# Kernel optimization log

Measured on AMD Instinct MI355X. Metric: run time of the kernel, lower is better.

Reference implementation:

```python
import jax, jax.numpy as jnp
import numpy as np

NUM_POINTS = 4
MAX_LEVELS = 2


def _bilinear(img, gx, gy, align_corners):
    # img: [C,H,W]; gx,gy: [P] normalized coords in [-1,1]; zero padding (torch grid_sample)
    C, H, W = img.shape
    if align_corners:
        ix = (gx + 1.0) * 0.5 * (W - 1)
        iy = (gy + 1.0) * 0.5 * (H - 1)
    else:
        ix = ((gx + 1.0) * W - 1.0) * 0.5
        iy = ((gy + 1.0) * H - 1.0) * 0.5
    x0 = jnp.floor(ix)
    y0 = jnp.floor(iy)
    wx1 = ix - x0
    wy1 = iy - y0

    def corner(xf, yf, w):
        xi = xf.astype(jnp.int32)
        yi = yf.astype(jnp.int32)
        valid = (xi >= 0) & (xi < W) & (yi >= 0) & (yi < H)
        v = img[:, jnp.clip(yi, 0, H - 1), jnp.clip(xi, 0, W - 1)]  # [C,P]
        return v * (w * valid)[None, :]

    return (corner(x0, y0, (1 - wx1) * (1 - wy1))
            + corner(x0 + 1, y0, wx1 * (1 - wy1))
            + corner(x0, y0 + 1, (1 - wx1) * wy1)
            + corner(x0 + 1, y0 + 1, wx1 * wy1))


_sample_ac = jax.vmap(lambda im, a, b: _bilinear(im, a, b, True))   # warp_affine path
_sample = jax.vmap(lambda im, a, b: _bilinear(im, a, b, False))     # MSDeformAttn path


def _warp_affine(src, M):
    # torch F.affine_grid + F.grid_sample, align_corners=True; src [N,C,H,W], M [N,2,3]
    N, C, H, W = src.shape
    ys = jnp.linspace(-1.0, 1.0, H)
    xs = jnp.linspace(-1.0, 1.0, W)
    gy, gx = jnp.meshgrid(ys, xs, indexing='ij')
    base = jnp.stack([gx.ravel(), gy.ravel(), jnp.ones(H * W, src.dtype)], 0)  # [3,HW]
    grid = jnp.einsum('nij,jp->nip', M, base)  # [N,2,HW]
    return _sample_ac(src, grid[:, 0], grid[:, 1]).reshape(N, C, H, W)


def setup_inputs() -> dict:
    key = jax.random.key(0)
    k = jax.random.split(key, 6)
    B, C, H, W = 2, 256, 100, 252
    x = jax.random.normal(k[0], (4, C, H, W), jnp.float32)
    record_len = jnp.full((B,), 2, dtype=jnp.int32)
    eye = jnp.array([[1.0, 0.0, 0.0], [0.0, 1.0, 0.0]], jnp.float32)
    pairwise_t_matrix = eye + 0.05 * jax.random.normal(k[1], (B, 2, 2, 2, 3), jnp.float32)
    w_off = 0.02 * jax.random.normal(k[2], (C, MAX_LEVELS * NUM_POINTS * 2), jnp.float32)
    b_off = 0.01 * jax.random.normal(k[3], (MAX_LEVELS * NUM_POINTS * 2,), jnp.float32)
    w_attn = 0.02 * jax.random.normal(k[4], (C, MAX_LEVELS * NUM_POINTS), jnp.float32)
    b_attn = 0.01 * jax.random.normal(k[5], (MAX_LEVELS * NUM_POINTS,), jnp.float32)
    return {"x": x, "record_len": record_len, "pairwise_t_matrix": pairwise_t_matrix,
            "w_off": w_off, "b_off": b_off, "w_attn": w_attn, "b_attn": b_attn}


def reference(x, record_len, pairwise_t_matrix, w_off, b_off, w_attn, b_attn):
    rl = [int(v) for v in np.asarray(record_len)]
    C, H, W = x.shape[1:]
    HW = H * W
    # get_reference_points(dim='2d'): pixel centers normalized to (0,1)
    rx = (jnp.arange(W, dtype=x.dtype) + 0.5) / W
    ry = (jnp.arange(H, dtype=x.dtype) + 0.5) / H
    gy, gx = jnp.meshgrid(ry, rx, indexing='ij')
    ref = jnp.stack([gx.ravel(), gy.ravel()], -1)  # [HW,2]
    norm = jnp.array([W, H], dtype=x.dtype)  # offset_normalizer = (W,H) per level
    outs = []
    start = 0
    for b, n in enumerate(rl):
        xx = x[start:start + n]
        start += n
        warped = _warp_affine(xx, pairwise_t_matrix[b, 0, :n])  # [n,C,H,W]
        q = warped[0].reshape(C, HW).T  # query = first agent, [HW,C]
        off = (q @ w_off + b_off).reshape(HW, MAX_LEVELS, NUM_POINTS, 2)[:, :n]  # [HW,n,P,2]
        aw = (q @ w_attn + b_attn).reshape(HW, MAX_LEVELS, NUM_POINTS)[:, :n]
        aw = jax.nn.softmax(aw.reshape(HW, n * NUM_POINTS), axis=-1).reshape(HW, n, NUM_POINTS)
        loc = ref[:, None, None, :] + off / norm  # sampling locations in (0,1)
        grid = 2.0 * loc - 1.0  # [HW,n,P,2]
        gxs = grid[..., 0].transpose(1, 0, 2).reshape(n, HW * NUM_POINTS)
        gys = grid[..., 1].transpose(1, 0, 2).reshape(n, HW * NUM_POINTS)
        sampled = _sample(warped, gxs, gys).reshape(n, C, HW, NUM_POINTS)
        out = jnp.einsum('lcqp,qlp->cq', sampled, aw)  # weighted sum over levels*points
        outs.append(out.reshape(1, C, H, W))
    return jnp.concatenate(outs, 0)
```

## Files before the change

### kernel.cpp

```cpp
#include <hip/hip_runtime.h>
#include <stdint.h>

#define CCH 256
#define NCP 128
#define HH  100
#define WW  252
#define HWSZ (HH*WW)
#define NIMG 4
#define NB   2
#define LP   8

#define TW 64
#define TH 4
#define HLO 2
#define PAIRS_BLOCK 16
#define TILESX ((WW + TW - 1)/TW)
#define TILESY (HH/TH)

#define WRW 70
#define WRH 5
#define WPL 384
#define WISS 6

typedef float vf2 __attribute__((ext_vector_type(2)));

__device__ __forceinline__ uint32_t f2bf(float a) {
  uint32_t u = __float_as_uint(a);
  u += 0x7fffu + ((u >> 16) & 1u);
  return u >> 16;
}
__device__ __forceinline__ float lof(uint32_t u) {
  return __uint_as_float(u << 16);
}
__device__ __forceinline__ float hif(uint32_t u) {
  return __uint_as_float(u & 0xffff0000u);
}
__device__ __forceinline__ vf2 unpk(uint32_t u) {
  vf2 r; r.x = lof(u); r.y = hif(u); return r;
}

__device__ __forceinline__ int swz100(int bid) {
  int xcd = bid & 7, idx = bid >> 3;
  const int q = 100/8, r = 100%8;
  return (xcd < r) ? xcd*(q+1) + idx : r*(q+1) + (xcd-r)*q + idx;
}

__device__ __forceinline__ void gload_lds_u(const uint32_t* g, uint32_t* l) {
  auto gp = reinterpret_cast<const uint32_t __attribute__((address_space(1)))*>(
      reinterpret_cast<uintptr_t>(g));
  auto lp = reinterpret_cast<uint32_t __attribute__((address_space(3)))*>(
      reinterpret_cast<uintptr_t>(l));
  __builtin_amdgcn_global_load_lds(gp, lp, 4, 0, 0);
}

__global__ __launch_bounds__(256) void warp_kernel(
    const float* __restrict__ x, const float* __restrict__ tmat,
    uint32_t* __restrict__ wpk)
{
  int tid = threadIdx.x;
  int y  = swz100(blockIdx.x);
  int g  = blockIdx.y;
  int cc = blockIdx.z;
  bool valid = tid < WW;
  int xo = min(tid, WW-1);
  int b = g >> 1, i = g & 1;
  const float* M = tmat + (size_t)(b*4 + i)*6;
  float m00=M[0], m01=M[1], m02=M[2], m10=M[3], m11=M[4], m12=M[5];
  float gx = -1.0f + 2.0f*(float)xo/(float)(WW-1);
  float gy = -1.0f + 2.0f*(float)y /(float)(HH-1);
  float sx = m00*gx + m01*gy + m02;
  float sy = m10*gx + m11*gy + m12;
  float ix = (sx + 1.0f)*0.5f*(float)(WW-1);
  float iy = (sy + 1.0f)*0.5f*(float)(HH-1);
  float x0f = floorf(ix), y0f = floorf(iy);
  float wx1 = ix - x0f,  wy1 = iy - y0f;
  int x0 = (int)x0f, y0 = (int)y0f;
  int x1 = x0 + 1,  y1 = y0 + 1;
  float v0x = (x0 >= 0 && x0 < WW) ? 1.f : 0.f;
  float v1x = (x1 >= 0 && x1 < WW) ? 1.f : 0.f;
  float v0y = (y0 >= 0 && y0 < HH) ? 1.f : 0.f;
  float v1y = (y1 >= 0 && y1 < HH) ? 1.f : 0.f;
  float w0 = (1.f-wx1)*(1.f-wy1)*v0x*v0y;
  float w1 = wx1*(1.f-wy1)*v1x*v0y;
  float w2 = (1.f-wx1)*wy1*v0x*v1y;
  float w3 = wx1*wy1*v1x*v1y;
  int yc0 = min(max(y0,0),HH-1), yc1 = min(max(y1,0),HH-1);
  int xb  = min(max(x0,0),WW-2);
  bool cnd = (x0 == xb);

  const float* src = x + ((size_t)g*CCH + (size_t)cc*32)*HWSZ;
  uint32_t vo_t = (uint32_t)(yc0*WW + xb)*4u;
  uint32_t vo_b = (uint32_t)(yc1*WW + xb)*4u;
  uint32_t* dst = wpk + ((size_t)g*NCP + (size_t)cc*PAIRS_BLOCK)*HWSZ + y*WW + xo;

  vf2 d[4][4];

  #define WLD(p) do {                                                        \
    uint32_t co = (uint32_t)(2*(p))*(HWSZ*4u);                               \
    asm volatile("global_load_dwordx2 %0, %1, %2"                            \
      : "=v"(d[(p)&3][0]) : "v"(vo_t + co), "s"(src));                       \
    asm volatile("global_load_dwordx2 %0, %1, %2"                            \
      : "=v"(d[(p)&3][1]) : "v"(vo_b + co), "s"(src));                       \
    asm volatile("global_load_dwordx2 %0, %1, %2"                            \
      : "=v"(d[(p)&3][2]) : "v"(vo_t + co + HWSZ*4u), "s"(src));             \
    asm volatile("global_load_dwordx2 %0, %1, %2"                            \
      : "=v"(d[(p)&3][3]) : "v"(vo_b + co + HWSZ*4u), "s"(src));             \
  } while (0)

  #define WCP(p) do {                                                        \
    vf2 t0 = d[(p)&3][0], b0 = d[(p)&3][1];                                  \
    vf2 t1 = d[(p)&3][2], b1 = d[(p)&3][3];                                  \
    float va0 = cnd ? t0.x : t0.y, vb0 = cnd ? t0.y : t0.x;                  \
    float vc0 = cnd ? b0.x : b0.y, vd0 = cnd ? b0.y : b0.x;                  \
    float va1 = cnd ? t1.x : t1.y, vb1 = cnd ? t1.y : t1.x;                  \
    float vc1 = cnd ? b1.x : b1.y, vd1 = cnd ? b1.y : b1.x;                  \
    float v0 = va0*w0 + vb0*w1 + vc0*w2 + vd0*w3;                            \
    float v1 = va1*w0 + vb1*w1 + vc1*w2 + vd1*w3;                            \
    if (valid) dst[(size_t)(p)*HWSZ] = f2bf(v0) | (f2bf(v1) << 16);          \
  } while (0)

  WLD(0); WLD(1); WLD(2); WLD(3);
  #pragma unroll
  for (int p = 0; p < PAIRS_BLOCK; ++p) {
    if      (p == 0)  { asm volatile("s_waitcnt vmcnt(12)" ::: "memory"); }
    else if (p == 1)  { asm volatile("s_waitcnt vmcnt(13)" ::: "memory"); }
    else if (p == 2)  { asm volatile("s_waitcnt vmcnt(14)" ::: "memory"); }
    else if (p <= 12) { asm volatile("s_waitcnt vmcnt(15)" ::: "memory"); }
    else if (p == 13) { asm volatile("s_waitcnt vmcnt(11)" ::: "memory"); }
    else if (p == 14) { asm volatile("s_waitcnt vmcnt(7)"  ::: "memory"); }
    else              { asm volatile("s_waitcnt vmcnt(3)"  ::: "memory"); }
    __builtin_amdgcn_sched_barrier(0);
    WCP(p);
    if (p + 4 < PAIRS_BLOCK) WLD(p + 4);
  }
  #undef WLD
  #undef WCP
}

__global__ __launch_bounds__(256) void b1_kernel(
    const uint32_t* __restrict__ wpk,
    const float* __restrict__ w_off,  const float* __restrict__ b_off,
    const float* __restrict__ w_attn, const float* __restrict__ b_attn,
    float* __restrict__ taps)
{
  __shared__ float red[3][64][25];
  int tid   = threadIdx.x;
  int lpx   = tid & 63;
  int slice = tid >> 6;
  int pix   = blockIdx.x * 64 + lpx;
  int b     = blockIdx.y;
  bool valid = pix < HWSZ;
  int pxc = valid ? pix : (HWSZ-1);
  const uint32_t* q = wpk + ((size_t)(2*b)*NCP + (size_t)slice*32)*HWSZ + pxc;
  float acc[24];
  #pragma unroll
  for (int j=0;j<24;++j) acc[j] = 0.f;
  for (int cp=0; cp<32; ++cp) {
    uint32_t u = q[(size_t)cp*HWSZ];
    float qlo = lof(u), qhi = hif(u);
    int cg = slice*64 + 2*cp;
    #pragma unroll
    for (int j=0;j<16;++j) acc[j]    += qlo * w_off[cg*16+j]  + qhi * w_off[(cg+1)*16+j];
    #pragma unroll
    for (int j=0;j<8;++j)  acc[16+j] += qlo * w_attn[cg*8+j]  + qhi * w_attn[(cg+1)*8+j];
  }
  if (slice > 0) {
    #pragma unroll
    for (int j=0;j<24;++j) red[slice-1][lpx][j] = acc[j];
  }
  __syncthreads();
  if (slice == 0 && valid) {
    #pragma unroll
    for (int s=0;s<3;++s)
      #pragma unroll
      for (int j=0;j<24;++j) acc[j] += red[s][lpx][j];
    #pragma unroll
    for (int j=0;j<16;++j) acc[j]    += b_off[j];
    #pragma unroll
    for (int j=0;j<8;++j)  acc[16+j] += b_attn[j];
    float m = acc[16];
    #pragma unroll
    for (int j=1;j<8;++j) m = fmaxf(m, acc[16+j]);
    float e[8]; float s = 0.f;
    #pragma unroll
    for (int j=0;j<8;++j){ e[j] = __expf(acc[16+j]-m); s += e[j]; }
    float inv = 1.0f/s;
    int px = pix % WW, py = pix / WW;
    float* t = taps + (size_t)b*24*HWSZ + pix;
    #pragma unroll
    for (int k=0;k<LP;++k) {
      t[(size_t)k*HWSZ]      = (float)px + acc[2*k];
      t[(size_t)(8+k)*HWSZ]  = (float)py + acc[2*k+1];
      t[(size_t)(16+k)*HWSZ] = e[k]*inv;
    }
  }
}

__global__ __launch_bounds__(256) void b2_kernel(
    const uint32_t* __restrict__ wpk, const float* __restrict__ taps,
    float* __restrict__ out)
{
  __shared__ uint32_t lds[4*2*2*WPL];
  int tid  = threadIdx.x;
  int lane = tid & 63, wid = tid >> 6;
  int s100 = swz100(blockIdx.x);
  int tx   = s100 / TILESY;
  int ty   = s100 - tx*TILESY;
  int b    = blockIdx.y;
  int pbase = blockIdx.z * PAIRS_BLOCK;
  int tx0 = tx * TW;
  int ty0 = ty * TH;
  int px = tx0 + lane;
  int py = ty0 + wid;
  bool valid = (px < WW);
  int pxc = min(px, WW-1);
  int pix = py*WW + pxc;
  int cx0 = tx0 - HLO;
  int ry0 = py - HLO;

  const float* t = taps + (size_t)b*24*HWSZ + pix;
  float wgt[LP][4];
  int   lidx[LP];
  bool fastall = true;
  #pragma unroll
  for (int k=0;k<LP;++k) {
    float ix = t[(size_t)k*HWSZ];
    float iy = t[(size_t)(8+k)*HWSZ];
    float aw = t[(size_t)(16+k)*HWSZ];
    float x0f = floorf(ix), y0f = floorf(iy);
    float wx1 = ix-x0f, wy1 = iy-y0f;
    int x0=(int)x0f, y0=(int)y0f;
    float v0x = (x0   >= 0 && x0   < WW) ? 1.f : 0.f;
    float v1x = (x0+1 >= 0 && x0+1 < WW) ? 1.f : 0.f;
    float v0y = (y0   >= 0 && y0   < HH) ? 1.f : 0.f;
    float v1y = (y0+1 >= 0 && y0+1 < HH) ? 1.f : 0.f;
    wgt[k][0] = (1.f-wx1)*(1.f-wy1)*v0x*v0y*aw;
    wgt[k][1] = wx1*(1.f-wy1)*v1x*v0y*aw;
    wgt[k][2] = (1.f-wx1)*wy1*v0x*v1y*aw;
    wgt[k][3] = wx1*wy1*v1x*v1y*aw;
    bool f = (x0 >= cx0) && (x0 <= cx0+WRW-2) && (y0 >= ry0) && (y0 <= ry0+WRH-2);
    fastall = fastall && f;
    int li = (y0-ry0)*WRW + (x0-cx0);
    lidx[k] = f ? li : 0;
  }

  int goff[WISS];
  #pragma unroll
  for (int n=0;n<WISS;++n) {
    int e = n*64 + lane;
    int r = e / WRW;
    int c = e - r*WRW;
    int gy = min(max(ry0 + r, 0), HH-1);
    int gx = min(max(cx0 + c, 0), WW-1);
    goff[n] = gy*WW + gx;
  }

  const uint32_t* g0 = wpk + ((size_t)(2*b+0)*NCP + pbase)*HWSZ;
  const uint32_t* g1 = wpk + ((size_t)(2*b+1)*NCP + pbase)*HWSZ;
  uint32_t* wb = &lds[wid*2*2*WPL];

  #define B2_ISSUE(ph, buf) do {                                           \
    const uint32_t* gA = g0 + (size_t)(ph)*HWSZ;                           \
    const uint32_t* gB = g1 + (size_t)(ph)*HWSZ;                           \
    uint32_t* lb = wb + (buf)*2*WPL;                                       \
    _Pragma("unroll")                                                      \
    for (int n=0;n<WISS;++n) gload_lds_u(gA + goff[n], lb + n*64);         \
    _Pragma("unroll")                                                      \
    for (int n=0;n<WISS;++n) gload_lds_u(gB + goff[n], lb + WPL + n*64);   \
  } while (0)

  #define B2_COMPUTE(ph, buf) do {                                         \
    const uint32_t* L0 = wb + (buf)*2*WPL;                                 \
    const uint32_t* L1 = L0 + WPL;                                         \
    vf2 v = {0.f, 0.f};                                                    \
    if (fastall) {                                                         \
      _Pragma("unroll")                                                    \
      for (int k=0;k<LP;++k) {                                             \
        const uint32_t* L = (k<4) ? L0 : L1;                               \
        int id = lidx[k];                                                  \
        v += unpk(L[id])*wgt[k][0];                                        \
        v += unpk(L[id+1])*wgt[k][1];                                      \
        v += unpk(L[id+WRW])*wgt[k][2];                                    \
        v += unpk(L[id+WRW+1])*wgt[k][3];                                  \
      }                                                                    \
    } else {                                                               \
      _Pragma("unroll")                                                    \
      for (int k=0;k<LP;++k) {                                             \
        float ix = t[(size_t)k*HWSZ];                                      \
        float iy = t[(size_t)(8+k)*HWSZ];                                  \
        int x0=(int)floorf(ix), y0=(int)floorf(iy);                        \
        int xc0=min(max(x0,0),WW-1), xc1=min(max(x0+1,0),WW-1);            \
        int yc0=min(max(y0,0),HH-1), yc1=min(max(y0+1,0),HH-1);            \
        const uint32_t* p = (k<4) ? (g0 + (size_t)(ph)*HWSZ)               \
                                  : (g1 + (size_t)(ph)*HWSZ);              \
        v += unpk(p[yc0*WW+xc0])*wgt[k][0];                                \
        v += unpk(p[yc0*WW+xc1])*wgt[k][1];                                \
        v += unpk(p[yc1*WW+xc0])*wgt[k][2];                                \
        v += unpk(p[yc1*WW+xc1])*wgt[k][3];                                \
      }                                                                    \
    }                                                                      \
    if (valid) {                                                           \
      int c = 2*(pbase + (ph));                                            \
      out[((size_t)b*CCH + c  )*HWSZ + pix] = v.x;                         \
      out[((size_t)b*CCH + c+1)*HWSZ + pix] = v.y;                         \
    }                                                                      \
  } while (0)

  B2_ISSUE(0, 0);
  B2_ISSUE(1, 1);
  #pragma unroll
  for (int ph = 0; ph < PAIRS_BLOCK; ++ph) {
    if (ph == 0) {
      asm volatile("s_waitcnt vmcnt(12)" ::: "memory");
    } else if (ph < PAIRS_BLOCK-1) {
      asm volatile("s_waitcnt vmcnt(14)" ::: "memory");
    } else {
      asm volatile("s_waitcnt vmcnt(2)" ::: "memory");
    }
    __builtin_amdgcn_sched_barrier(0);
    B2_COMPUTE(ph, ph & 1);
    if (ph + 2 < PAIRS_BLOCK) B2_ISSUE(ph + 2, ph & 1);
  }
  #undef B2_ISSUE
  #undef B2_COMPUTE
}

extern "C" void kernel_launch(void* const* d_in, const int* in_sizes, int n_in,
                              void* d_out, int out_size, void* d_ws, size_t ws_size,
                              hipStream_t stream) {
  const float* x      = (const float*)d_in[0];
  const float* tmat   = (const float*)d_in[2];
  const float* w_off  = (const float*)d_in[3];
  const float* b_off  = (const float*)d_in[4];
  const float* w_attn = (const float*)d_in[5];
  const float* b_attn = (const float*)d_in[6];
  float* out = (float*)d_out;

  uint32_t* wpk = (uint32_t*)d_ws;
  float*    taps = (float*)((char*)d_ws +
                     (size_t)NIMG*NCP*HWSZ*sizeof(uint32_t));

  warp_kernel<<<dim3(HH, NIMG, NCP/PAIRS_BLOCK), 256, 0, stream>>>(x, tmat, wpk);
  b1_kernel<<<dim3((HWSZ+63)/64, NB), 256, 0, stream>>>(wpk, w_off, b_off,
                                                        w_attn, b_attn, taps);
  b2_kernel<<<dim3(TILESX*TILESY, NB, NCP/PAIRS_BLOCK), 256, 0, stream>>>(wpk, taps, out);
}
```

Baseline: 124.5 us.

## Stage source row bands into LDS with async global-to-LDS loads in warp kernel

The warp kernel now computes, per output row, the band of source rows the affine sampling can touch. When that band fits in 16 rows, each channel's band is copied into a double-buffered LDS tile with 16-byte global_load_lds transfers, and the bilinear taps are read from LDS. Otherwise it falls back to direct global gathers. This replaces scattered per-thread dwordx2 gathers with coalesced row copies, at the cost of two block barriers per channel and more bytes loaded per channel. The helper swizzle is generalized to take N.

```diff
diff --git a/kernel.cpp b/kernel.cpp
--- a/kernel.cpp
+++ b/kernel.cpp
@@ -22,6 +22,9 @@
 #define WPL 384
 #define WISS 6
 
+#define BMAX 16
+#define RSL  256
+
 typedef float vf2 __attribute__((ext_vector_type(2)));
 
 __device__ __forceinline__ uint32_t f2bf(float a) {
@@ -39,9 +42,9 @@
   vf2 r; r.x = lof(u); r.y = hif(u); return r;
 }
 
-__device__ __forceinline__ int swz100(int bid) {
+__device__ __forceinline__ int swzN(int bid, int N) {
   int xcd = bid & 7, idx = bid >> 3;
-  const int q = 100/8, r = 100%8;
+  int q = N >> 3, r = N & 7;
   return (xcd < r) ? xcd*(q+1) + idx : r*(q+1) + (xcd-r)*q + idx;
 }
 
@@ -52,13 +55,22 @@
       reinterpret_cast<uintptr_t>(l));
   __builtin_amdgcn_global_load_lds(gp, lp, 4, 0, 0);
 }
+__device__ __forceinline__ void gload_lds16f(const float* g, float* l) {
+  auto gp = reinterpret_cast<const uint32_t __attribute__((address_space(1)))*>(
+      reinterpret_cast<uintptr_t>(g));
+  auto lp = reinterpret_cast<uint32_t __attribute__((address_space(3)))*>(
+      reinterpret_cast<uintptr_t>(l));
+  __builtin_amdgcn_global_load_lds(gp, lp, 16, 0, 0);
+}
 
 __global__ __launch_bounds__(256) void warp_kernel(
     const float* __restrict__ x, const float* __restrict__ tmat,
     uint32_t* __restrict__ wpk)
 {
-  int tid = threadIdx.x;
-  int y  = swz100(blockIdx.x);
+  __shared__ float lds[2][BMAX][RSL];
+  int tid  = threadIdx.x;
+  int lane = tid & 63, wid = tid >> 6;
+  int y  = swzN(blockIdx.x, HH);
   int g  = blockIdx.y;
   int cc = blockIdx.z;
   bool valid = tid < WW;
@@ -85,56 +97,67 @@
   float w2 = (1.f-wx1)*wy1*v0x*v1y;
   float w3 = wx1*wy1*v1x*v1y;
   int yc0 = min(max(y0,0),HH-1), yc1 = min(max(y1,0),HH-1);
-  int xb  = min(max(x0,0),WW-2);
-  bool cnd = (x0 == xb);
+  int xc0 = min(max(x0,0),WW-1), xc1 = min(max(x1,0),WW-1);
+
+  float iyA = ((-m00*0.f - m10 + m11*gy + m12) + 1.0f)*0.5f*(float)(HH-1);
+  float iyB = (( m10 + m11*gy + m12) + 1.0f)*0.5f*(float)(HH-1);
+  float mnf = fminf(iyA, iyB), mxf = fmaxf(iyA, iyB);
+  int band0 = max(0, (int)floorf(mnf));
+  int btop  = min(HH-1, (int)ceilf(mxf) + 1);
+  bool fits = (btop - band0 + 1) <= BMAX;
 
   const float* src = x + ((size_t)g*CCH + (size_t)cc*32)*HWSZ;
-  uint32_t vo_t = (uint32_t)(yc0*WW + xb)*4u;
-  uint32_t vo_b = (uint32_t)(yc1*WW + xb)*4u;
   uint32_t* dst = wpk + ((size_t)g*NCP + (size_t)cc*PAIRS_BLOCK)*HWSZ + y*WW + xo;
 
-  vf2 d[4][4];
-
-  #define WLD(p) do {                                                        \
-    uint32_t co = (uint32_t)(2*(p))*(HWSZ*4u);                               \
-    asm volatile("global_load_dwordx2 %0, %1, %2"                            \
-      : "=v"(d[(p)&3][0]) : "v"(vo_t + co), "s"(src));                       \
-    asm volatile("global_load_dwordx2 %0, %1, %2"                            \
-      : "=v"(d[(p)&3][1]) : "v"(vo_b + co), "s"(src));                       \
-    asm volatile("global_load_dwordx2 %0, %1, %2"                            \
-      : "=v"(d[(p)&3][2]) : "v"(vo_t + co + HWSZ*4u), "s"(src));             \
-    asm volatile("global_load_dwordx2 %0, %1, %2"                            \
-      : "=v"(d[(p)&3][3]) : "v"(vo_b + co + HWSZ*4u), "s"(src));             \
-  } while (0)
-
-  #define WCP(p) do {                                                        \
-    vf2 t0 = d[(p)&3][0], b0 = d[(p)&3][1];                                  \
-    vf2 t1 = d[(p)&3][2], b1 = d[(p)&3][3];                                  \
-    float va0 = cnd ? t0.x : t0.y, vb0 = cnd ? t0.y : t0.x;                  \
-    float vc0 = cnd ? b0.x : b0.y, vd0 = cnd ? b0.y : b0.x;                  \
-    float va1 = cnd ? t1.x : t1.y, vb1 = cnd ? t1.y : t1.x;                  \
-    float vc1 = cnd ? b1.x : b1.y, vd1 = cnd ? b1.y : b1.x;                  \
-    float v0 = va0*w0 + vb0*w1 + vc0*w2 + vd0*w3;                            \
-    float v1 = va1*w0 + vb1*w1 + vc1*w2 + vd1*w3;                            \
-    if (valid) dst[(size_t)(p)*HWSZ] = f2bf(v0) | (f2bf(v1) << 16);          \
-  } while (0)
-
-  WLD(0); WLD(1); WLD(2); WLD(3);
-  #pragma unroll
-  for (int p = 0; p < PAIRS_BLOCK; ++p) {
-    if      (p == 0)  { asm volatile("s_waitcnt vmcnt(12)" ::: "memory"); }
-    else if (p == 1)  { asm volatile("s_waitcnt vmcnt(13)" ::: "memory"); }
-    else if (p == 2)  { asm volatile("s_waitcnt vmcnt(14)" ::: "memory"); }
-    else if (p <= 12) { asm volatile("s_waitcnt vmcnt(15)" ::: "memory"); }
-    else if (p == 13) { asm volatile("s_waitcnt vmcnt(11)" ::: "memory"); }
-    else if (p == 14) { asm volatile("s_waitcnt vmcnt(7)"  ::: "memory"); }
-    else              { asm volatile("s_waitcnt vmcnt(3)"  ::: "memory"); }
-    __builtin_amdgcn_sched_barrier(0);
-    WCP(p);
-    if (p + 4 < PAIRS_BLOCK) WLD(p + 4);
-  }
-  #undef WLD
-  #undef WCP
+  if (fits) {
+    int colb = min(lane*4, WW-4);
+    int r0 = yc0 - band0, r1 = yc1 - band0;
+    int grow[4];
+    #pragma unroll
+    for (int k=0;k<4;++k) grow[k] = min(band0 + wid + 4*k, HH-1);
+
+    #define WISSUE(p) do {                                                   \
+      const float* pl = src + (size_t)(p)*HWSZ;                              \
+      _Pragma("unroll")                                                      \
+      for (int k=0;k<4;++k)                                                  \
+        gload_lds16f(pl + grow[k]*WW + colb, &lds[(p)&1][wid+4*k][0]);       \
+    } while (0)
+
+    float vprev = 0.f;
+    WISSUE(0);
+    WISSUE(1);
+    #pragma unroll
+    for (int p = 0; p < 32; ++p) {
+      if      (p == 31)           { asm volatile("s_waitcnt vmcnt(0)" ::: "memory"); }
+      else if ((p & 1) || p == 0) { asm volatile("s_waitcnt vmcnt(4)" ::: "memory"); }
+      else                        { asm volatile("s_waitcnt vmcnt(5)" ::: "memory"); }
+      __builtin_amdgcn_sched_barrier(0);
+      asm volatile("s_barrier" ::: "memory");
+      const float* L = &lds[p&1][0][0];
+      float l00 = L[r0*RSL + xc0], l01 = L[r0*RSL + xc1];
+      float l10 = L[r1*RSL + xc0], l11 = L[r1*RSL + xc1];
+      float v = l00*w0 + l01*w1 + l10*w2 + l11*w3;
+      if (p & 1) {
+        if (valid) dst[(size_t)(p>>1)*HWSZ] = f2bf(vprev) | (f2bf(v) << 16);
+      } else {
+        vprev = v;
+      }
+      asm volatile("s_barrier" ::: "memory");
+      if (p + 2 < 32) WISSUE(p + 2);
+    }
+    #undef WISSUE
+  } else {
+    int o00 = yc0*WW + xc0, o01 = yc0*WW + xc1;
+    int o10 = yc1*WW + xc0, o11 = yc1*WW + xc1;
+    #pragma unroll 4
+    for (int p = 0; p < PAIRS_BLOCK; ++p) {
+      const float* p0 = src + (size_t)(2*p)*HWSZ;
+      const float* p1 = p0 + HWSZ;
+      float v0 = p0[o00]*w0 + p0[o01]*w1 + p0[o10]*w2 + p0[o11]*w3;
+      float v1 = p1[o00]*w0 + p1[o01]*w1 + p1[o10]*w2 + p1[o11]*w3;
+      if (valid) dst[(size_t)p*HWSZ] = f2bf(v0) | (f2bf(v1) << 16);
+    }
+  }
 }
 
 __global__ __launch_bounds__(256) void b1_kernel(
@@ -203,7 +226,7 @@
   __shared__ uint32_t lds[4*2*2*WPL];
   int tid  = threadIdx.x;
   int lane = tid & 63, wid = tid >> 6;
-  int s100 = swz100(blockIdx.x);
+  int s100 = swzN(blockIdx.x, TILESX*TILESY);
   int tx   = s100 / TILESY;
   int ty   = s100 - tx*TILESY;
   int b    = blockIdx.y;
```

New measurement: 163.3 us. +31.2%, slower.
